# Performance work log

Measured on AMD Instinct MI355X. Metric: run time of the kernel, lower is better.

Reference implementation:

```python
import jax, jax.numpy as jnp
import numpy as np

B, S, D, H, L = 8, 2048, 512, 8, 5
DK = D // H
SP = S - L + 1  # number of local windows


def setup_inputs() -> dict:
    key = jax.random.key(0)
    ks = jax.random.split(key, 5)
    scale = 1.0 / np.sqrt(D).astype(np.float32)
    return {
        "query": jax.random.normal(ks[0], (B, S, D), dtype=jnp.float32),
        "key": jax.random.normal(ks[1], (B, S, D), dtype=jnp.float32),
        "value": jax.random.normal(ks[2], (B, S, D), dtype=jnp.float32),
        "W0": jax.random.normal(ks[3], (D, D), dtype=jnp.float32) * scale,
        "b0": jnp.zeros((D,), dtype=jnp.float32),
        "Wout": jax.random.normal(ks[4], (D, D), dtype=jnp.float32) * scale,
        "bout": jnp.zeros((D,), dtype=jnp.float32),
    }


def _local_agg(x, weighted):
    # x: (B, S, D). Sliding-window aggregation over windows of length L.
    # scores[b, t, s] = <x[b, t+L-1], x[b, s]> / sqrt(D)  -- per the source:
    # matmul(x[:, L-1:], x^T) / sqrt(d_model)
    scores = jnp.einsum("btd,bsd->bts", x[:, L - 1:], x) / (float(D) ** 0.5)
    idx = jnp.arange(SP)[:, None] + jnp.arange(L)[None, :]  # (SP, L)
    # per-window softmax over the L local scores
    w = jax.nn.softmax(jnp.take_along_axis(scores, idx[None, :, :], axis=-1), axis=-1)  # (B, SP, L)
    win = x[:, idx]  # (B, SP, L, D) gathered windows
    if weighted:
        win = w[..., None] * win
    return jnp.sum(win, axis=2)  # (B, SP, D)


def reference(query, key, value, W0, b0, Wout, bout):
    # Bug-faithful: the source overwrites the weighted query with the raw
    # windows (`query = q_list`), so query windows are summed UNweighted;
    # key windows use the local softmax weights.
    q = _local_agg(query, weighted=False)  # (B, SP, D)
    k = _local_agg(key, weighted=True)     # (B, SP, D)
    v = value[:, L - 1:] @ W0 + b0         # linears[0], aligned to SP positions

    def heads(t):  # (B, SP, D) -> (B, H, SP, DK)
        return t.reshape(t.shape[0], t.shape[1], H, DK).transpose(0, 2, 1, 3)

    qh, kh, vh = heads(q), heads(k), heads(v)
    att = jax.nn.softmax(jnp.einsum("bhtd,bhsd->bhts", qh, kh) / (float(DK) ** 0.5), axis=-1)
    x = jnp.einsum("bhts,bhsd->bhtd", att, vh)  # (B, H, SP, DK)
    x = x.transpose(0, 2, 1, 3).reshape(q.shape[0], SP, D)
    return x @ Wout + bout  # linears[-1]
```

## Files before the change

### kernel.cpp

```cpp
#include <hip/hip_runtime.h>
#include <hip/hip_bf16.h>
#include <hip/hip_fp16.h>

#define B_ 8
#define S_ 2048
#define D_ 512
#define H_ 8
#define L_ 5
#define DK_ 64
#define SP_ 2044
#define SPAD_ 2048

typedef _Float16 f16_t;
typedef _Float16 f16x4 __attribute__((ext_vector_type(4)));
typedef _Float16 f16x8 __attribute__((ext_vector_type(8)));
typedef __fp16 fp16x2_b __attribute__((ext_vector_type(2)));
typedef float f32x4 __attribute__((ext_vector_type(4)));

static __device__ __forceinline__ f32x4 mfma16(f16x8 a, f16x8 b, f32x4 c) {
    return __builtin_amdgcn_mfma_f32_16x16x32_f16(a, b, c, 0, 0, 0);
}

union PK4 { f16x4 v; fp16x2_b h[2]; };

__global__ __launch_bounds__(256) void k_convert_w(
    const float* __restrict__ W0, const float* __restrict__ Wout,
    f16_t* __restrict__ WT0, f16_t* __restrict__ WT1) {
    int idx = blockIdx.x * 256 + threadIdx.x;
    int which = idx >> 18;
    int e = idx & 0x3FFFF;
    int k = e >> 9, n = e & 511;
    const float* W = which ? Wout : W0;
    f16_t* WT = which ? WT1 : WT0;
    WT[n * 512 + k] = (f16_t)W[k * 512 + n];
}

__global__ __launch_bounds__(256) void k_prep(
    const float* __restrict__ Qin, const float* __restrict__ Kin,
    f16_t* __restrict__ qh, f16_t* __restrict__ kh) {
    const int lane = threadIdx.x & 63;
    const int wid = threadIdx.x >> 6;
    const int gw = blockIdx.x * 4 + wid;
    const int b = gw >> 11;
    const int t = gw & 2047;
    const float* qb = Qin + (size_t)b * S_ * D_;
    const float* kb = Kin + (size_t)b * S_ * D_;
    const int d0 = lane * 8;

    float qs[8];
    float kl[5][8];
#pragma unroll
    for (int e = 0; e < 8; e++) qs[e] = 0.f;
#pragma unroll
    for (int l = 0; l < L_; l++) {
        int row = t + l; row = row < 2047 ? row : 2047;
        const float4* qp = (const float4*)(qb + (size_t)row * D_ + d0);
        float4 a = qp[0], c = qp[1];
        qs[0] += a.x; qs[1] += a.y; qs[2] += a.z; qs[3] += a.w;
        qs[4] += c.x; qs[5] += c.y; qs[6] += c.z; qs[7] += c.w;
        const float4* kp = (const float4*)(kb + (size_t)row * D_ + d0);
        float4 ka = kp[0], kc = kp[1];
        kl[l][0] = ka.x; kl[l][1] = ka.y; kl[l][2] = ka.z; kl[l][3] = ka.w;
        kl[l][4] = kc.x; kl[l][5] = kc.y; kl[l][6] = kc.z; kl[l][7] = kc.w;
    }
    float dot[5];
#pragma unroll
    for (int l = 0; l < 5; l++) {
        float d = 0.f;
#pragma unroll
        for (int e = 0; e < 8; e++) d += kl[4][e] * kl[l][e];
        dot[l] = d;
    }
#pragma unroll
    for (int m = 32; m; m >>= 1) {
#pragma unroll
        for (int l = 0; l < 5; l++) dot[l] += __shfl_xor(dot[l], m, 64);
    }
    const float sc = 0.044194173824159216f;
    float mx = dot[0];
#pragma unroll
    for (int l = 1; l < 5; l++) mx = fmaxf(mx, dot[l]);
    float w[5], sum = 0.f;
#pragma unroll
    for (int l = 0; l < 5; l++) { w[l] = __expf((dot[l] - mx) * sc); sum += w[l]; }
    float inv = 1.f / sum;
    float ks[8];
#pragma unroll
    for (int e = 0; e < 8; e++) {
        float v = 0.f;
#pragma unroll
        for (int l = 0; l < 5; l++) v += w[l] * kl[l][e];
        ks[e] = v * inv;
    }
    const int h = d0 >> 6, dk = d0 & 63;
    const size_t ob = ((size_t)(b * H_ + h) * SPAD_ + t) * DK_ + dk;
    const float qscale = 0.125f * 1.4426950408889634f;
    f16x8 qpk, kpk;
#pragma unroll
    for (int e = 0; e < 8; e++) {
        qpk[e] = (f16_t)(qs[e] * qscale);
        kpk[e] = (f16_t)ks[e];
    }
    *(f16x8*)(qh + ob) = qpk;
    *(f16x8*)(kh + ob) = kpk;
}

template <int MODE>
__global__ __launch_bounds__(256) void k_gemm(
    const void* __restrict__ Aptr, const f16_t* __restrict__ WT,
    const float* __restrict__ bias, void* __restrict__ Cptr) {
    __shared__ alignas(16) char smem[40960];
    const int tid = threadIdx.x, lane = tid & 63, wid = tid >> 6;
    const int mt = blockIdx.x >> 2, nt = blockIdx.x & 3;
    const int m0 = mt * 128, n0 = nt * 128;
    const int l15 = lane & 15, lg = lane >> 4;
    f32x4 acc[2][8] = {};

    const float* a0src = nullptr;
    const f16_t* a1src0 = nullptr, *a1src1 = nullptr;
    if (MODE == 0) {
        const float* A = (const float*)Aptr;
        int r = tid >> 1, cb = (tid & 1) * 16;
        int rp = m0 + r, b = rp >> 11, t = rp & 2047;
        int vrow = t + 4; vrow = vrow < 2047 ? vrow : 2047;
        a0src = A + ((size_t)b * 2048 + vrow) * 512 + cb;
    } else {
        const f16_t* A = (const f16_t*)Aptr;
        int r0 = tid >> 2, off0 = (tid & 3) * 8;
        int r1 = (tid + 256) >> 2, off1 = (tid & 3) * 8;
        a1src0 = A + (size_t)(m0 + r0) * 512 + off0;
        a1src1 = A + (size_t)(m0 + r1) * 512 + off1;
    }
    const int bnl0 = tid >> 2, bko0 = (tid & 3) * 8;
    const int bnl1 = (tid + 256) >> 2;
    const f16_t* bsrc0 = WT + (size_t)(n0 + bnl0) * 512 + bko0;
    const f16_t* bsrc1 = WT + (size_t)(n0 + bnl1) * 512 + bko0;

    float4 fa[4];
    uint4 ua0, ua1, ub0, ub1;
    if (MODE == 0) {
#pragma unroll
        for (int j = 0; j < 4; j++) fa[j] = *(const float4*)(a0src + j * 4);
    } else {
        ua0 = *(const uint4*)a1src0;
        ua1 = *(const uint4*)a1src1;
    }
    ub0 = *(const uint4*)bsrc0;
    ub1 = *(const uint4*)bsrc1;

    for (int kt = 0; kt < 16; ++kt) {
        const int cur = kt & 1;
        f16_t (*Asm)[40] = (f16_t(*)[40])(smem + cur * 10240);
        f16_t (*Bsm)[40] = (f16_t(*)[40])(smem + 20480 + cur * 10240);
        if (MODE == 0) {
            int r = tid >> 1, cb = (tid & 1) * 16;
            f16x8 p0, p1;
            p0[0] = (f16_t)fa[0].x; p0[1] = (f16_t)fa[0].y; p0[2] = (f16_t)fa[0].z; p0[3] = (f16_t)fa[0].w;
            p0[4] = (f16_t)fa[1].x; p0[5] = (f16_t)fa[1].y; p0[6] = (f16_t)fa[1].z; p0[7] = (f16_t)fa[1].w;
            p1[0] = (f16_t)fa[2].x; p1[1] = (f16_t)fa[2].y; p1[2] = (f16_t)fa[2].z; p1[3] = (f16_t)fa[2].w;
            p1[4] = (f16_t)fa[3].x; p1[5] = (f16_t)fa[3].y; p1[6] = (f16_t)fa[3].z; p1[7] = (f16_t)fa[3].w;
            *(f16x8*)&Asm[r][cb] = p0;
            *(f16x8*)&Asm[r][cb + 8] = p1;
        } else {
            int r0 = tid >> 2, r1 = (tid + 256) >> 2, off = (tid & 3) * 8;
            *(uint4*)&Asm[r0][off] = ua0;
            *(uint4*)&Asm[r1][off] = ua1;
        }
        *(uint4*)&Bsm[bnl0][bko0] = ub0;
        *(uint4*)&Bsm[bnl1][bko0] = ub1;
        if (kt < 15) {
            const int k0n = (kt + 1) * 32;
            if (MODE == 0) {
#pragma unroll
                for (int j = 0; j < 4; j++) fa[j] = *(const float4*)(a0src + k0n + j * 4);
            } else {
                ua0 = *(const uint4*)(a1src0 + k0n);
                ua1 = *(const uint4*)(a1src1 + k0n);
            }
            ub0 = *(const uint4*)(bsrc0 + k0n);
            ub1 = *(const uint4*)(bsrc1 + k0n);
        }
        __syncthreads();
        f16x8 af[2], bfr[8];
#pragma unroll
        for (int i = 0; i < 2; i++) af[i] = *(const f16x8*)&Asm[wid * 32 + i * 16 + l15][lg * 8];
#pragma unroll
        for (int c = 0; c < 8; c++) bfr[c] = *(const f16x8*)&Bsm[c * 16 + l15][lg * 8];
        __builtin_amdgcn_s_setprio(1);
#pragma unroll
        for (int i = 0; i < 2; i++) {
#pragma unroll
            for (int c = 0; c < 8; c++) acc[i][c] = mfma16(af[i], bfr[c], acc[i][c]);
        }
        __builtin_amdgcn_s_setprio(0);
    }

    if (MODE == 0) {
        __syncthreads();
        f16_t (*Csm)[136] = (f16_t(*)[136])smem;
#pragma unroll
        for (int i = 0; i < 2; i++) {
#pragma unroll
            for (int c = 0; c < 8; c++) {
                int col = n0 + c * 16 + l15;
                float bv = bias[col];
                f16x4 pk;
#pragma unroll
                for (int r = 0; r < 4; r++) pk[r] = (f16_t)(acc[i][c][r] + bv);
                *(f16x4*)&Csm[c * 16 + l15][wid * 32 + i * 16 + lg * 4] = pk;
            }
        }
        __syncthreads();
        const int b = m0 >> 11, t0 = m0 & 2047;
        const int cl = tid >> 1, mo = (tid & 1) * 64;
        const int h = (n0 + cl) >> 6, dk = (n0 + cl) & 63;
        f16_t* dst = (f16_t*)Cptr + ((size_t)(b * H_ + h) * DK_ + dk) * SPAD_ + t0 + mo;
#pragma unroll
        for (int j = 0; j < 8; j++)
            *(uint4*)(dst + j * 8) = *(const uint4*)&Csm[cl][mo + j * 8];
    } else {
#pragma unroll
        for (int i = 0; i < 2; i++) {
#pragma unroll
            for (int c = 0; c < 8; c++) {
#pragma unroll
                for (int r = 0; r < 4; r++) {
                    int row = m0 + wid * 32 + i * 16 + lg * 4 + r;
                    int col = n0 + c * 16 + l15;
                    float v = acc[i][c][r] + bias[col];
                    int b = row >> 11, t = row & 2047;
                    if (t < SP_) {
                        float* outp = (float*)Cptr;
                        outp[((size_t)b * SP_ + t) * 512 + col] = v;
                    }
                }
            }
        }
    }
}

__global__ __launch_bounds__(256) void k_attn(
    const f16_t* __restrict__ qh, const f16_t* __restrict__ kh,
    const f16_t* __restrict__ vhT, f16_t* __restrict__ xatt) {
    __shared__ alignas(16) f16_t Ksm[2][64][68];
    __shared__ alignas(16) f16_t Vsm[2][64][68];
    __shared__ alignas(16) f16_t Plds[4][2][16][68];
    const int tid = threadIdx.x, lane = tid & 63, wid = tid >> 6;
    const int vb = ((blockIdx.x & 7) << 7) | (blockIdx.x >> 3);
    const int bh = vb >> 4, qt = vb & 15;
    const f16_t* Q = qh + (size_t)bh * SPAD_ * DK_;
    const f16_t* K = kh + (size_t)bh * SPAD_ * DK_;
    const f16_t* VT = vhT + (size_t)bh * DK_ * SPAD_;
    const int l15 = lane & 15, lg = lane >> 4;
    const int qbase = qt * 128 + wid * 32;

    f16x8 qf[2][2];
#pragma unroll
    for (int h = 0; h < 2; h++)
#pragma unroll
        for (int kf = 0; kf < 2; kf++)
            qf[h][kf] = *(const f16x8*)(Q + (size_t)(qbase + h * 16 + l15) * DK_ + kf * 32 + lg * 8);

    f16x8 ones;
#pragma unroll
    for (int e = 0; e < 8; e++) ones[e] = (f16_t)1.0f;
    const f32x4 cinit = {-12.f, -12.f, -12.f, -12.f};

    f32x4 acc[2][4] = {};
    f32x4 rsacc[2] = {};

    const int sr = tid >> 3, so = (tid & 7) * 8;
    const f16_t* kg0 = K + (size_t)sr * DK_ + so;
    const f16_t* kg1 = K + (size_t)(sr + 32) * DK_ + so;
    const f16_t* vg0 = VT + (size_t)sr * SPAD_ + so;
    const f16_t* vg1 = VT + (size_t)(sr + 32) * SPAD_ + so;

    uint4 rk0 = *(const uint4*)kg0;
    uint4 rk1 = *(const uint4*)kg1;
    uint4 rv0 = *(const uint4*)vg0;
    uint4 rv1 = *(const uint4*)vg1;

    for (int t = 0; t < 32; ++t) {
        const int cur = t & 1;
        *(uint4*)&Ksm[cur][sr][so]      = rk0;
        *(uint4*)&Ksm[cur][sr + 32][so] = rk1;
        *(uint4*)&Vsm[cur][sr][so]      = rv0;
        *(uint4*)&Vsm[cur][sr + 32][so] = rv1;
        if (t < 31) {
            const int nxt = (t + 1) << 6;
            rk0 = *(const uint4*)(kg0 + (size_t)nxt * DK_);
            rk1 = *(const uint4*)(kg1 + (size_t)nxt * DK_);
            rv0 = *(const uint4*)(vg0 + nxt);
            rv1 = *(const uint4*)(vg1 + nxt);
        }
        __syncthreads();

        f32x4 Sv[2][4];
        __builtin_amdgcn_s_setprio(1);
#pragma unroll
        for (int n = 0; n < 4; n++) {
            f16x8 kb0 = *(const f16x8*)&Ksm[cur][n * 16 + l15][lg * 8];
            f16x8 kb1 = *(const f16x8*)&Ksm[cur][n * 16 + l15][32 + lg * 8];
#pragma unroll
            for (int h = 0; h < 2; h++) {
                f32x4 s = mfma16(kb0, qf[h][0], cinit);
                s = mfma16(kb1, qf[h][1], s);
                Sv[h][n] = s;
            }
        }
        __builtin_amdgcn_s_setprio(0);
        if (t == 31) {
#pragma unroll
            for (int n = 0; n < 4; n++) {
                int kb = 1984 + n * 16 + lg * 4;
#pragma unroll
                for (int r = 0; r < 4; r++)
                    if (kb + r >= SP_) { Sv[0][n][r] = -1e30f; Sv[1][n][r] = -1e30f; }
            }
        }
#pragma unroll
        for (int h = 0; h < 2; h++) {
#pragma unroll
            for (int n = 0; n < 4; n++) {
                float e0 = __builtin_amdgcn_exp2f(Sv[h][n][0]);
                float e1 = __builtin_amdgcn_exp2f(Sv[h][n][1]);
                float e2 = __builtin_amdgcn_exp2f(Sv[h][n][2]);
                float e3 = __builtin_amdgcn_exp2f(Sv[h][n][3]);
                PK4 pk;
                pk.h[0] = __builtin_amdgcn_cvt_pkrtz(e0, e1);
                pk.h[1] = __builtin_amdgcn_cvt_pkrtz(e2, e3);
                *(f16x4*)&Plds[wid][h][l15][n * 16 + lg * 4] = pk.v;
            }
        }
        __builtin_amdgcn_s_setprio(1);
#pragma unroll
        for (int ko = 0; ko < 2; ko++) {
            f16x8 pa0 = *(const f16x8*)&Plds[wid][0][l15][ko * 32 + lg * 8];
            f16x8 pa1 = *(const f16x8*)&Plds[wid][1][l15][ko * 32 + lg * 8];
            rsacc[0] = mfma16(ones, pa0, rsacc[0]);
            rsacc[1] = mfma16(ones, pa1, rsacc[1]);
#pragma unroll
            for (int c = 0; c < 4; c++) {
                f16x8 vb2 = *(const f16x8*)&Vsm[cur][c * 16 + l15][ko * 32 + lg * 8];
                acc[0][c] = mfma16(vb2, pa0, acc[0][c]);
                acc[1][c] = mfma16(vb2, pa1, acc[1][c]);
            }
        }
        __builtin_amdgcn_s_setprio(0);
    }

    const int b = bh >> 3, hh = bh & 7;
#pragma unroll
    for (int h = 0; h < 2; h++) {
        float inv = 1.f / rsacc[h][0];
#pragma unroll
        for (int c = 0; c < 4; c++) {
            f16x4 pk;
#pragma unroll
            for (int r = 0; r < 4; r++) pk[r] = (f16_t)(acc[h][c][r] * inv);
            *(f16x4*)&Plds[wid][h][l15][c * 16 + lg * 4] = pk;
        }
    }
    const int qr = lane >> 2, dc = (lane & 3) * 16;
#pragma unroll
    for (int h = 0; h < 2; h++) {
        f16_t* dst = xatt + ((size_t)b * SPAD_ + qbase + h * 16 + qr) * D_ + hh * DK_ + dc;
        *(uint4*)dst = *(const uint4*)&Plds[wid][h][qr][dc];
        *(uint4*)(dst + 8) = *(const uint4*)&Plds[wid][h][qr][dc + 8];
    }
}

extern "C" void kernel_launch(void* const* d_in, const int* in_sizes, int n_in,
                              void* d_out, int out_size, void* d_ws, size_t ws_size,
                              hipStream_t stream) {
    const float* query = (const float*)d_in[0];
    const float* key   = (const float*)d_in[1];
    const float* value = (const float*)d_in[2];
    const float* W0    = (const float*)d_in[3];
    const float* b0    = (const float*)d_in[4];
    const float* Wout  = (const float*)d_in[5];
    const float* bout  = (const float*)d_in[6];
    float* out = (float*)d_out;

    char* w = (char*)d_ws;
    const size_t SZ = (size_t)B_ * H_ * SPAD_ * DK_ * sizeof(f16_t);
    f16_t* qh   = (f16_t*)w; w += SZ;
    f16_t* kh   = (f16_t*)w; w += SZ;
    f16_t* vhT  = (f16_t*)w; w += SZ;
    f16_t* xatt = (f16_t*)w; w += SZ;
    f16_t* WT0  = (f16_t*)w; w += (size_t)512 * 512 * sizeof(f16_t);
    f16_t* WT1  = (f16_t*)w; w += (size_t)512 * 512 * sizeof(f16_t);

    k_convert_w<<<2048, 256, 0, stream>>>(W0, Wout, WT0, WT1);
    k_prep<<<4096, 256, 0, stream>>>(query, key, qh, kh);
    k_gemm<0><<<512, 256, 0, stream>>>((const void*)value, WT0, b0, (void*)vhT);
    k_attn<<<1024, 256, 0, stream>>>(qh, kh, vhT, xatt);
    k_gemm<1><<<512, 256, 0, stream>>>((const void*)xatt, WT1, bout, (void*)out);
}
```

Baseline: 178.8 us.

## Rewrite attention with 32x32 MFMA, register-resident P via permlane swaps

The attention kernel moves from 16x16x32 to 32x32x16 MFMA tiles, with each wave handling 64 queries and each block 256, so the grid halves. The softmax probabilities stay in registers and are rearranged into B-operand layout with permlane32 swaps, replacing the LDS round-trip. Row sums come from fdot2 instead of a ones-matrix MFMA. This cuts LDS traffic and matrix instructions per tile, in exchange for higher register pressure (launch bounds now ask for 2 blocks) and fewer blocks in flight.

```diff
diff --git a/kernel.cpp b/kernel.cpp
--- a/kernel.cpp
+++ b/kernel.cpp
@@ -16,12 +16,30 @@
 typedef _Float16 f16x8 __attribute__((ext_vector_type(8)));
 typedef __fp16 fp16x2_b __attribute__((ext_vector_type(2)));
 typedef float f32x4 __attribute__((ext_vector_type(4)));
+typedef float f32x16 __attribute__((ext_vector_type(16)));
+typedef unsigned int u32;
 
 static __device__ __forceinline__ f32x4 mfma16(f16x8 a, f16x8 b, f32x4 c) {
     return __builtin_amdgcn_mfma_f32_16x16x32_f16(a, b, c, 0, 0, 0);
 }
+static __device__ __forceinline__ f32x16 mfma32(f16x8 a, f16x8 b, f32x16 c) {
+    return __builtin_amdgcn_mfma_f32_32x32x16_f16(a, b, c, 0, 0, 0);
+}
 
 union PK4 { f16x4 v; fp16x2_b h[2]; };
+union U32H2 { u32 u; fp16x2_b h; };
+union FRAG { uint4 u; f16x8 f; };
+
+static __device__ __forceinline__ void swap32(u32 a, u32 b, u32& r0, u32& r1, int hi) {
+#if __has_builtin(__builtin_amdgcn_permlane32_swap)
+    auto r = __builtin_amdgcn_permlane32_swap(a, b, false, false);
+    r0 = r[0]; r1 = r[1];
+#else
+    u32 t = __shfl_xor(hi ? a : b, 32, 64);
+    r0 = hi ? t : a;
+    r1 = hi ? b : t;
+#endif
+}
 
 __global__ __launch_bounds__(256) void k_convert_w(
     const float* __restrict__ W0, const float* __restrict__ Wout,
@@ -127,9 +145,9 @@
     } else {
         const f16_t* A = (const f16_t*)Aptr;
         int r0 = tid >> 2, off0 = (tid & 3) * 8;
-        int r1 = (tid + 256) >> 2, off1 = (tid & 3) * 8;
+        int r1 = (tid + 256) >> 2;
         a1src0 = A + (size_t)(m0 + r0) * 512 + off0;
-        a1src1 = A + (size_t)(m0 + r1) * 512 + off1;
+        a1src1 = A + (size_t)(m0 + r1) * 512 + off0;
     }
     const int bnl0 = tid >> 2, bko0 = (tid & 3) * 8;
     const int bnl1 = (tid + 256) >> 2;
@@ -239,35 +257,35 @@
     }
 }
 
-__global__ __launch_bounds__(256) void k_attn(
+__global__ __launch_bounds__(256, 2) void k_attn(
     const f16_t* __restrict__ qh, const f16_t* __restrict__ kh,
     const f16_t* __restrict__ vhT, f16_t* __restrict__ xatt) {
     __shared__ alignas(16) f16_t Ksm[2][64][68];
     __shared__ alignas(16) f16_t Vsm[2][64][68];
-    __shared__ alignas(16) f16_t Plds[4][2][16][68];
     const int tid = threadIdx.x, lane = tid & 63, wid = tid >> 6;
-    const int vb = ((blockIdx.x & 7) << 7) | (blockIdx.x >> 3);
-    const int bh = vb >> 4, qt = vb & 15;
+    const int l31 = lane & 31, hi = lane >> 5, hi8 = hi * 8;
+    const int vb = ((blockIdx.x & 7) << 6) | (blockIdx.x >> 3);
+    const int bh = vb >> 3, qt = vb & 7;
     const f16_t* Q = qh + (size_t)bh * SPAD_ * DK_;
     const f16_t* K = kh + (size_t)bh * SPAD_ * DK_;
     const f16_t* VT = vhT + (size_t)bh * DK_ * SPAD_;
-    const int l15 = lane & 15, lg = lane >> 4;
-    const int qbase = qt * 128 + wid * 32;
-
-    f16x8 qf[2][2];
-#pragma unroll
-    for (int h = 0; h < 2; h++)
-#pragma unroll
-        for (int kf = 0; kf < 2; kf++)
-            qf[h][kf] = *(const f16x8*)(Q + (size_t)(qbase + h * 16 + l15) * DK_ + kf * 32 + lg * 8);
-
-    f16x8 ones;
-#pragma unroll
-    for (int e = 0; e < 8; e++) ones[e] = (f16_t)1.0f;
-    const f32x4 cinit = {-12.f, -12.f, -12.f, -12.f};
-
-    f32x4 acc[2][4] = {};
-    f32x4 rsacc[2] = {};
+    const int qw = qt * 256 + wid * 64;
+
+    f16x8 qf[2][4];
+#pragma unroll
+    for (int qg = 0; qg < 2; qg++)
+#pragma unroll
+        for (int kf = 0; kf < 4; kf++)
+            qf[qg][kf] = *(const f16x8*)(Q + (size_t)(qw + qg * 32 + l31) * DK_ + kf * 16 + hi8);
+
+    f32x16 cinit;
+#pragma unroll
+    for (int i = 0; i < 16; i++) cinit[i] = -12.f;
+
+    f32x16 acc[2][2] = {};
+    float rsa[2] = {0.f, 0.f}, rsb[2] = {0.f, 0.f};
+    u32 pk[2][2][8];
+    U32H2 one2; one2.u = 0x3C003C00u;
 
     const int sr = tid >> 3, so = (tid & 7) * 8;
     const f16_t* kg0 = K + (size_t)sr * DK_ + so;
@@ -295,78 +313,105 @@
         }
         __syncthreads();
 
-        f32x4 Sv[2][4];
-        __builtin_amdgcn_s_setprio(1);
-#pragma unroll
-        for (int n = 0; n < 4; n++) {
-            f16x8 kb0 = *(const f16x8*)&Ksm[cur][n * 16 + l15][lg * 8];
-            f16x8 kb1 = *(const f16x8*)&Ksm[cur][n * 16 + l15][32 + lg * 8];
-#pragma unroll
-            for (int h = 0; h < 2; h++) {
-                f32x4 s = mfma16(kb0, qf[h][0], cinit);
-                s = mfma16(kb1, qf[h][1], s);
-                Sv[h][n] = s;
-            }
-        }
-        __builtin_amdgcn_s_setprio(0);
-        if (t == 31) {
-#pragma unroll
-            for (int n = 0; n < 4; n++) {
-                int kb = 1984 + n * 16 + lg * 4;
-#pragma unroll
-                for (int r = 0; r < 4; r++)
-                    if (kb + r >= SP_) { Sv[0][n][r] = -1e30f; Sv[1][n][r] = -1e30f; }
-            }
-        }
-#pragma unroll
-        for (int h = 0; h < 2; h++) {
-#pragma unroll
-            for (int n = 0; n < 4; n++) {
-                float e0 = __builtin_amdgcn_exp2f(Sv[h][n][0]);
-                float e1 = __builtin_amdgcn_exp2f(Sv[h][n][1]);
-                float e2 = __builtin_amdgcn_exp2f(Sv[h][n][2]);
-                float e3 = __builtin_amdgcn_exp2f(Sv[h][n][3]);
-                PK4 pk;
-                pk.h[0] = __builtin_amdgcn_cvt_pkrtz(e0, e1);
-                pk.h[1] = __builtin_amdgcn_cvt_pkrtz(e2, e3);
-                *(f16x4*)&Plds[wid][h][l15][n * 16 + lg * 4] = pk.v;
-            }
-        }
-        __builtin_amdgcn_s_setprio(1);
-#pragma unroll
-        for (int ko = 0; ko < 2; ko++) {
-            f16x8 pa0 = *(const f16x8*)&Plds[wid][0][l15][ko * 32 + lg * 8];
-            f16x8 pa1 = *(const f16x8*)&Plds[wid][1][l15][ko * 32 + lg * 8];
-            rsacc[0] = mfma16(ones, pa0, rsacc[0]);
-            rsacc[1] = mfma16(ones, pa1, rsacc[1]);
-#pragma unroll
-            for (int c = 0; c < 4; c++) {
-                f16x8 vb2 = *(const f16x8*)&Vsm[cur][c * 16 + l15][ko * 32 + lg * 8];
-                acc[0][c] = mfma16(vb2, pa0, acc[0][c]);
-                acc[1][c] = mfma16(vb2, pa1, acc[1][c]);
-            }
-        }
-        __builtin_amdgcn_s_setprio(0);
-    }
-
+#pragma unroll
+        for (int kr = 0; kr < 2; ++kr) {
+            f32x16 sv0 = cinit, sv1 = cinit;
+            __builtin_amdgcn_s_setprio(1);
+#pragma unroll
+            for (int kf = 0; kf < 4; ++kf) {
+                f16x8 a = *(const f16x8*)&Ksm[cur][kr * 32 + l31][kf * 16 + hi8];
+                sv0 = mfma32(a, qf[0][kf], sv0);
+                sv1 = mfma32(a, qf[1][kf], sv1);
+            }
+            __builtin_amdgcn_s_setprio(0);
+            if (t == 31 && kr == 1) {
+#pragma unroll
+                for (int r = 12; r < 16; ++r) {
+                    sv0[r] = hi ? -1e30f : sv0[r];
+                    sv1[r] = hi ? -1e30f : sv1[r];
+                }
+            }
+#pragma unroll
+            for (int j = 0; j < 8; ++j) {
+                float a0 = __builtin_amdgcn_exp2f(sv0[2 * j]);
+                float a1 = __builtin_amdgcn_exp2f(sv0[2 * j + 1]);
+                U32H2 c0; c0.h = __builtin_amdgcn_cvt_pkrtz(a0, a1);
+                pk[0][kr][j] = c0.u;
+                float b0 = __builtin_amdgcn_exp2f(sv1[2 * j]);
+                float b1 = __builtin_amdgcn_exp2f(sv1[2 * j + 1]);
+                U32H2 c1; c1.h = __builtin_amdgcn_cvt_pkrtz(b0, b1);
+                pk[1][kr][j] = c1.u;
+#if __has_builtin(__builtin_amdgcn_fdot2)
+                if (j & 1) {
+                    rsb[0] = __builtin_amdgcn_fdot2(c0.h, one2.h, rsb[0], false);
+                    rsb[1] = __builtin_amdgcn_fdot2(c1.h, one2.h, rsb[1], false);
+                } else {
+                    rsa[0] = __builtin_amdgcn_fdot2(c0.h, one2.h, rsa[0], false);
+                    rsa[1] = __builtin_amdgcn_fdot2(c1.h, one2.h, rsa[1], false);
+                }
+#else
+                if (j & 1) { rsb[0] += a0 + a1; rsb[1] += b0 + b1; }
+                else       { rsa[0] += a0 + a1; rsa[1] += b0 + b1; }
+#endif
+            }
+        }
+
+#pragma unroll
+        for (int kc = 0; kc < 4; ++kc) {
+            const int kr = kc >> 1, al = (kc & 1) * 4;
+            FRAG p0, p1;
+            {
+                u32 m0, m1, m2, m3;
+                swap32(pk[0][kr][al],     pk[0][kr][al + 2], m0, m2, hi);
+                swap32(pk[0][kr][al + 1], pk[0][kr][al + 3], m1, m3, hi);
+                p0.u = make_uint4(m0, m1, m2, m3);
+                swap32(pk[1][kr][al],     pk[1][kr][al + 2], m0, m2, hi);
+                swap32(pk[1][kr][al + 1], pk[1][kr][al + 3], m1, m3, hi);
+                p1.u = make_uint4(m0, m1, m2, m3);
+            }
+            __builtin_amdgcn_s_setprio(1);
+#pragma unroll
+            for (int dc = 0; dc < 2; ++dc) {
+                f16x8 v = *(const f16x8*)&Vsm[cur][dc * 32 + l31][kc * 16 + hi8];
+                acc[0][dc] = mfma32(v, p0.f, acc[0][dc]);
+                acc[1][dc] = mfma32(v, p1.f, acc[1][dc]);
+            }
+            __builtin_amdgcn_s_setprio(0);
+        }
+    }
+
+    float rs0 = rsa[0] + rsb[0];
+    float rs1 = rsa[1] + rsb[1];
+    rs0 += __shfl_xor(rs0, 32, 64);
+    rs1 += __shfl_xor(rs1, 32, 64);
+    const float inv[2] = {1.f / rs0, 1.f / rs1};
+
+    __syncthreads();
+    f16_t (*Osm)[68] = (f16_t(*)[68])&Ksm[0][0][0];
+#pragma unroll
+    for (int qg = 0; qg < 2; ++qg) {
+        const int row = wid * 64 + qg * 32 + l31;
+#pragma unroll
+        for (int dc = 0; dc < 2; ++dc) {
+#pragma unroll
+            for (int p = 0; p < 8; ++p) {
+                float e0 = acc[qg][dc][2 * p] * inv[qg];
+                float e1 = acc[qg][dc][2 * p + 1] * inv[qg];
+                U32H2 c; c.h = __builtin_amdgcn_cvt_pkrtz(e0, e1);
+                const int d = dc * 32 + 2 * (p & 1) + 8 * (p >> 1) + 4 * hi;
+                *(u32*)&Osm[row][d] = c.u;
+            }
+        }
+    }
+    __syncthreads();
     const int b = bh >> 3, hh = bh & 7;
 #pragma unroll
-    for (int h = 0; h < 2; h++) {
-        float inv = 1.f / rsacc[h][0];
-#pragma unroll
-        for (int c = 0; c < 4; c++) {
-            f16x4 pk;
-#pragma unroll
-            for (int r = 0; r < 4; r++) pk[r] = (f16_t)(acc[h][c][r] * inv);
-            *(f16x4*)&Plds[wid][h][l15][c * 16 + lg * 4] = pk;
-        }
-    }
-    const int qr = lane >> 2, dc = (lane & 3) * 16;
-#pragma unroll
-    for (int h = 0; h < 2; h++) {
-        f16_t* dst = xatt + ((size_t)b * SPAD_ + qbase + h * 16 + qr) * D_ + hh * DK_ + dc;
-        *(uint4*)dst = *(const uint4*)&Plds[wid][h][qr][dc];
-        *(uint4*)(dst + 8) = *(const uint4*)&Plds[wid][h][qr][dc + 8];
+    for (int ps = 0; ps < 8; ++ps) {
+        const int row = wid * 64 + ps * 8 + (lane >> 3);
+        const int dco = (lane & 7) * 8;
+        uint4 v = *(const uint4*)&Osm[row][dco];
+        f16_t* dst = xatt + ((size_t)b * SPAD_ + qt * 256 + row) * D_ + hh * DK_ + dco;
+        *(uint4*)dst = v;
     }
 }
 
@@ -394,6 +439,6 @@
     k_convert_w<<<2048, 256, 0, stream>>>(W0, Wout, WT0, WT1);
     k_prep<<<4096, 256, 0, stream>>>(query, key, qh, kh);
     k_gemm<0><<<512, 256, 0, stream>>>((const void*)value, WT0, b0, (void*)vhT);
-    k_attn<<<1024, 256, 0, stream>>>(qh, kh, vhT, xatt);
+    k_attn<<<512, 256, 0, stream>>>(qh, kh, vhT, xatt);
     k_gemm<1><<<512, 256, 0, stream>>>((const void*)xatt, WT1, bout, (void*)out);
 }
```

Result: faster. 154.2 us (-13.7%).
